# Performance work log

Measured on AMD Instinct MI355X. Metric: run time of the kernel, lower is better.

Reference implementation:

```python
import jax, jax.numpy as jnp
import numpy as np

B, T, N, FIN = 32, 12, 1024, 64
K, OUT_F = 3, 64


def setup_inputs() -> dict:
    key = jax.random.key(0)
    k1, k2, k3 = jax.random.split(key, 3)
    x = jax.random.normal(k1, (B, T, N, FIN), dtype=jnp.float32)
    A = jax.random.uniform(k2, (B, N, N), dtype=jnp.float32)
    # Xavier-uniform-like init for Theta [K, in_f, out_f]
    limit = float(np.sqrt(6.0 / (FIN + OUT_F)))
    Theta = jax.random.uniform(k3, (K, FIN, OUT_F), dtype=jnp.float32,
                               minval=-limit, maxval=limit)
    return {"x": x, "A": A, "Theta": Theta}


def reference(x, A, Theta):
    Bb, Tt, Nn, Fin = x.shape
    Kk = Theta.shape[0]
    I = jnp.broadcast_to(jnp.eye(Nn, dtype=x.dtype), (Bb, Nn, Nn))
    # lambda_max = max row-sum of A, clamped to >= 1
    lambda_max = jnp.maximum(jnp.max(jnp.sum(A, axis=-1), axis=-1), 1.0)
    L = 2.0 * A / lambda_max[:, None, None] - I  # scaled Laplacian surrogate [B,N,N]
    out = jnp.zeros((Bb, Tt, Nn, Theta.shape[-1]), dtype=x.dtype)
    T_prev2, T_prev = None, I
    for k in range(Kk):  # small fixed K-hop loop
        if k == 0:
            T_k = I
        elif k == 1:
            T_k = L
        else:
            T_k = 2.0 * jnp.einsum('bnm,bmp->bnp', L, T_prev) - T_prev2
        T_prev2, T_prev = T_prev, T_k
        rhs = jnp.einsum('btnf,fo->btno', x, Theta[k])   # feature transform
        out = out + jnp.einsum('bnm,btmo->btno', T_k, rhs)  # graph aggregation
    return jax.nn.relu(out)
```

## Files before the change

### kernel.cpp

```cpp
#include <hip/hip_runtime.h>

typedef unsigned short ushort_t;
typedef unsigned char uchar_t;
typedef __attribute__((ext_vector_type(8))) __bf16 bf16x8;
typedef __attribute__((ext_vector_type(4))) float f32x4;
typedef __attribute__((ext_vector_type(8))) unsigned short u16x8;
typedef __attribute__((ext_vector_type(8))) int i32x8;

#define NB 32
#define TT 12
#define NNODE 1024
#define FF 64
#define OO 64
#define TO 768

#define SCL_ONE 127
#define SCL_E   118

__device__ __forceinline__ unsigned short f2bf(float f) {
    unsigned u = __float_as_uint(f);
    u += 0x7FFFu + ((u >> 16) & 1u);
    return (unsigned short)(u >> 16);
}
__device__ __forceinline__ float bf2f(unsigned short h) {
    return __uint_as_float(((unsigned)h) << 16);
}
__device__ __forceinline__ unsigned char f2fp8(float f) {
    return (unsigned char)(__builtin_amdgcn_cvt_pk_fp8_f32(f, f, 0, false) & 0xff);
}

__device__ __forceinline__ void gload16(const void* g, void* l) {
    __builtin_amdgcn_global_load_lds(
        (const __attribute__((address_space(1))) unsigned int*)g,
        (__attribute__((address_space(3))) unsigned int*)l, 16, 0, 0);
}

__global__ void k_init(unsigned* lam) {
    if (threadIdx.x < NB) lam[threadIdx.x] = 0x3F800000u;
}

__global__ __launch_bounds__(256) void k_rowmax(const float* __restrict__ A,
                                                unsigned* __restrict__ lam) {
    const int b = blockIdx.x >> 4;
    const int chunk = blockIdx.x & 15;
    const int w = threadIdx.x >> 6, lane = threadIdx.x & 63;
    const float* Ab = A + (size_t)b * NNODE * NNODE;
    float mx = 0.0f;
    for (int r = 0; r < 16; ++r) {
        const float* rp = Ab + (size_t)(chunk * 64 + w * 16 + r) * NNODE;
        float s = 0.0f;
#pragma unroll
        for (int j = 0; j < 16; ++j) s += rp[lane + j * 64];
#pragma unroll
        for (int off = 32; off > 0; off >>= 1) s += __shfl_down(s, off, 64);
        if (lane == 0) mx = fmaxf(mx, s);
    }
    if (lane == 0) atomicMax(&lam[b], __float_as_uint(mx));
}

__global__ __launch_bounds__(256) void k_escale(const float* __restrict__ A,
                                                const unsigned* __restrict__ lam,
                                                uchar_t* __restrict__ E8) {
    const size_t idx = ((size_t)blockIdx.x * 256 + threadIdx.x) * 8;
    const int b = (int)(idx >> 20);
    const float scl = 1024.0f / __uint_as_float(lam[b]);
    const float4 v0 = *(const float4*)(A + idx);
    const float4 v1 = *(const float4*)(A + idx + 4);
    unsigned lo = 0, hi = 0;
    lo = (unsigned)__builtin_amdgcn_cvt_pk_fp8_f32(v0.x * scl, v0.y * scl, (int)lo, false);
    lo = (unsigned)__builtin_amdgcn_cvt_pk_fp8_f32(v0.z * scl, v0.w * scl, (int)lo, true);
    hi = (unsigned)__builtin_amdgcn_cvt_pk_fp8_f32(v1.x * scl, v1.y * scl, (int)hi, false);
    hi = (unsigned)__builtin_amdgcn_cvt_pk_fp8_f32(v1.z * scl, v1.w * scl, (int)hi, true);
    uint2 pk; pk.x = lo; pk.y = hi;
    *(uint2*)(E8 + idx) = pk;
}

__global__ void k_theta(const float* __restrict__ Th, ushort_t* __restrict__ Tht) {
    int tid = blockIdx.x * 256 + threadIdx.x;
    if (tid < 3 * 64 * 64) {
        int k = tid >> 12, rem = tid & 4095, o = rem >> 6, f = rem & 63;
        Tht[tid] = f2bf(Th[(k << 12) + (f << 6) + o]);
    }
}

__global__ __launch_bounds__(256) void k_feature(const float* __restrict__ x,
                                                 const ushort_t* __restrict__ Tht,
                                                 ushort_t* __restrict__ Pb,
                                                 ushort_t* __restrict__ Qc,
                                                 uchar_t* __restrict__ R2f8) {
    __shared__ ushort_t xt[128 * 64];
    __shared__ ushort_t tb[64 * 136];
    const int n0 = blockIdx.x * 128;
    const int t = blockIdx.y;
    const int b = blockIdx.z;
    const int tid = threadIdx.x;
    const int w = tid >> 6, lane = tid & 63, quad = lane >> 4, l15 = lane & 15;

    const float* xb = x + (((size_t)b * TT + t) * NNODE + n0) * FF;
#pragma unroll
    for (int i = 0; i < 8; ++i) {
        int q = i * 256 + tid;
        int row = q >> 4, fq = q & 15;
        const float4 v = *(const float4*)(xb + row * 64 + fq * 4);
        uint2 pk;
        pk.x = (unsigned)f2bf(v.x) | ((unsigned)f2bf(v.y) << 16);
        pk.y = (unsigned)f2bf(v.z) | ((unsigned)f2bf(v.w) << 16);
        *(uint2*)(xt + row * 64 + fq * 4) = pk;
    }
    __syncthreads();

    bf16x8 af[2][2];
#pragma unroll
    for (int rb = 0; rb < 2; ++rb)
#pragma unroll
        for (int ks = 0; ks < 2; ++ks)
            af[rb][ks] = *(const bf16x8*)(xt + (w * 32 + rb * 16 + l15) * 64 + ks * 32 + quad * 8);

    f32x4 acc[3][2][4];
#pragma unroll
    for (int k = 0; k < 3; ++k)
#pragma unroll
        for (int rb = 0; rb < 2; ++rb)
#pragma unroll
            for (int cb = 0; cb < 4; ++cb)
                acc[k][rb][cb] = (f32x4){0.f, 0.f, 0.f, 0.f};

#pragma unroll
    for (int k = 0; k < 3; ++k)
#pragma unroll
        for (int ks = 0; ks < 2; ++ks)
#pragma unroll
            for (int cb = 0; cb < 4; ++cb) {
                bf16x8 bfr = *(const bf16x8*)(Tht + ((size_t)(k * 64 + cb * 16 + l15)) * 64 + ks * 32 + quad * 8);
#pragma unroll
                for (int rb = 0; rb < 2; ++rb)
                    acc[k][rb][cb] = __builtin_amdgcn_mfma_f32_16x16x32_bf16(af[rb][ks], bfr, acc[k][rb][cb], 0, 0, 0);
            }

    ushort_t* Pbb = Pb + (((size_t)b * TT + t) * NNODE + n0) * OO;
#pragma unroll
    for (int rb = 0; rb < 2; ++rb)
#pragma unroll
        for (int cb = 0; cb < 4; ++cb)
#pragma unroll
            for (int r = 0; r < 4; ++r) {
                int n = w * 32 + rb * 16 + quad * 4 + r;
                int o = cb * 16 + l15;
                Pbb[(size_t)n * OO + o] = f2bf(acc[0][rb][cb][r] - acc[2][rb][cb][r]);
            }

    {
#pragma unroll
        for (int rb = 0; rb < 2; ++rb)
#pragma unroll
            for (int cb = 0; cb < 4; ++cb)
#pragma unroll
                for (int r = 0; r < 4; ++r) {
                    int nl = w * 32 + rb * 16 + quad * 4 + r;
                    int o = cb * 16 + l15;
                    tb[o * 136 + nl] = f2bf(acc[1][rb][cb][r] - 2.0f * acc[2][rb][cb][r]);
                }
        __syncthreads();
        int o = tid >> 2, seg = tid & 3;
        ushort_t* drow = Qc + ((size_t)b * TO + t * 64 + o) * NNODE + n0 + seg * 32;
        const ushort_t* srow = tb + o * 136 + seg * 32;
#pragma unroll
        for (int i = 0; i < 4; ++i)
            *(u16x8*)(drow + i * 8) = *(const u16x8*)(srow + i * 8);
        __syncthreads();
    }
    {
        char* tbc = (char*)tb;
#pragma unroll
        for (int rb = 0; rb < 2; ++rb)
#pragma unroll
            for (int cb = 0; cb < 4; ++cb)
#pragma unroll
                for (int r = 0; r < 4; ++r) {
                    int nl = w * 32 + rb * 16 + quad * 4 + r;
                    int o = cb * 16 + l15;
                    tbc[o * 144 + nl] = (char)f2fp8(acc[2][rb][cb][r]);
                }
        __syncthreads();
        int o = tid >> 2, seg = tid & 3;
        uchar_t* drow = R2f8 + ((size_t)b * TO + t * 64 + o) * NNODE + n0 + seg * 32;
        const char* srow = tbc + o * 144 + seg * 32;
        *(int4*)(drow) = *(const int4*)(srow);
        *(int4*)(drow + 16) = *(const int4*)(srow + 16);
    }
}

template <int MODE>
__global__ __launch_bounds__(256) void k_gemm8(const uchar_t* __restrict__ Aop, size_t aBS,
                                               const uchar_t* __restrict__ Bop, size_t bBS,
                                               const ushort_t* __restrict__ Qc,
                                               uchar_t* __restrict__ Zf8,
                                               ushort_t* __restrict__ Pbp,
                                               float* __restrict__ outp) {
    __shared__ __align__(16) uchar_t smem[34816];
    uchar_t* At = smem;
    uchar_t* Bt = smem + 16384;
    const int bid = blockIdx.x;
    const int xcd = bid & 7, y = bid >> 3;
    const int tile = y % 48;
    const int b = xcd + 8 * (y / 48);
    const int tm = (MODE == 1) ? (tile >> 3) : (tile / 6);
    const int tn = (MODE == 1) ? (tile & 7) : (tile % 6);
    const int m0 = tm * 128, n0 = tn * 128;
    const int tid = threadIdx.x;
    const int w = tid >> 6, lane = tid & 63, quad = lane >> 4, l15 = lane & 15;
    const int wr = w >> 1, wc = w & 1;
    const uchar_t* Ab = Aop + (size_t)b * aBS + (size_t)m0 * NNODE;
    const uchar_t* Bb = Bop + (size_t)b * bBS + (size_t)n0 * NNODE;

    int ldso[4];
    size_t goff[4];
#pragma unroll
    for (int i = 0; i < 4; ++i) {
        int slot = i * 256 + tid;
        int row = slot >> 3;
        int lc = (slot & 7) ^ (row & 7);
        ldso[i] = slot * 16;
        goff[i] = (size_t)row * NNODE + lc * 16;
    }

    f32x4 acc[4][4];
#pragma unroll
    for (int i = 0; i < 4; ++i)
#pragma unroll
        for (int j = 0; j < 4; ++j) acc[i][j] = (f32x4){0.f, 0.f, 0.f, 0.f};

    for (int kk = 0; kk < 8; ++kk) {
        const int k0 = kk << 7;
#pragma unroll
        for (int i = 0; i < 4; ++i) {
            gload16(Ab + k0 + goff[i], At + ldso[i]);
            gload16(Bb + k0 + goff[i], Bt + ldso[i]);
        }
        __syncthreads();
        i32x8 af[4], bfr[4];
#pragma unroll
        for (int i = 0; i < 4; ++i) {
            const int m = wr * 64 + i * 16 + l15;
            const int n = wc * 64 + i * 16 + l15;
            const int4 alo = *(const int4*)(At + m * 128 + (((quad << 1)) ^ (m & 7)) * 16);
            const int4 ahi = *(const int4*)(At + m * 128 + (((quad << 1) | 1) ^ (m & 7)) * 16);
            const int4 blo = *(const int4*)(Bt + n * 128 + (((quad << 1)) ^ (n & 7)) * 16);
            const int4 bhi = *(const int4*)(Bt + n * 128 + (((quad << 1) | 1) ^ (n & 7)) * 16);
            af[i] = (i32x8){alo.x, alo.y, alo.z, alo.w, ahi.x, ahi.y, ahi.z, ahi.w};
            bfr[i] = (i32x8){blo.x, blo.y, blo.z, blo.w, bhi.x, bhi.y, bhi.z, bhi.w};
        }
#pragma unroll
        for (int i = 0; i < 4; ++i)
#pragma unroll
            for (int j = 0; j < 4; ++j)
                acc[i][j] = __builtin_amdgcn_mfma_scale_f32_16x16x128_f8f6f4(
                    af[i], bfr[j], acc[i][j], 0, 0, 0, SCL_ONE, 0, SCL_E);
        __syncthreads();
    }

    if (MODE == 1) {
        ushort_t* tb = (ushort_t*)smem;
        const ushort_t* Qb = Qc + (size_t)b * TO * NNODE;
        uchar_t* Zb = Zf8 + (size_t)b * TO * NNODE;
#pragma unroll
        for (int i = 0; i < 4; ++i)
#pragma unroll
            for (int r = 0; r < 4; ++r) {
                const int cl = wr * 64 + i * 16 + quad * 4 + r;
                const int c = m0 + cl;
#pragma unroll
                for (int j = 0; j < 4; ++j) {
                    const int nl = wc * 64 + j * 16 + l15;
                    const size_t zi = (size_t)c * NNODE + n0 + nl;
                    const float z = bf2f(Qb[zi]) + 2.0f * acc[i][j][r];
                    Zb[zi] = f2fp8(z);
                    tb[nl * 136 + cl] = f2bf(z);
                }
            }
        __syncthreads();
        const int t0 = m0 >> 6;
        const int row = tid >> 1, half = tid & 1;
        ushort_t* prow = Pbp + (((size_t)b * TT + t0 + half) * NNODE + n0 + row) * OO;
        const ushort_t* srow = tb + row * 136 + half * 64;
#pragma unroll
        for (int s = 0; s < 8; ++s) {
            u16x8 pv = *(const u16x8*)(prow + s * 8);
            u16x8 zv = *(const u16x8*)(srow + s * 8);
            u16x8 rv;
#pragma unroll
            for (int e = 0; e < 8; ++e) rv[e] = f2bf(bf2f(pv[e]) - bf2f(zv[e]));
            *(u16x8*)(prow + s * 8) = rv;
        }
    } else {
#pragma unroll
        for (int i = 0; i < 4; ++i)
#pragma unroll
            for (int r = 0; r < 4; ++r) {
                const int n = m0 + wr * 64 + i * 16 + quad * 4 + r;
#pragma unroll
                for (int j = 0; j < 4; ++j) {
                    const int c = n0 + wc * 64 + j * 16 + l15;
                    const int t = c >> 6, o = c & 63;
                    const size_t id = (((size_t)b * TT + t) * NNODE + n) * OO + o;
                    outp[id] = fmaxf(bf2f(Pbp[id]) + acc[i][j][r], 0.0f);
                }
            }
    }
}

extern "C" void kernel_launch(void* const* d_in, const int* in_sizes, int n_in,
                              void* d_out, int out_size, void* d_ws, size_t ws_size,
                              hipStream_t stream) {
    const float* x = (const float*)d_in[0];
    const float* A = (const float*)d_in[1];
    const float* Th = (const float*)d_in[2];
    float* out = (float*)d_out;
    char* ws = (char*)d_ws;

    unsigned* lam = (unsigned*)ws;
    uchar_t* E8 = (uchar_t*)(ws + 256);
    uchar_t* R2f8 = E8 + (size_t)NB * NNODE * NNODE;
    uchar_t* Zf8 = R2f8 + (size_t)NB * TO * NNODE;
    ushort_t* Qc = (ushort_t*)(Zf8 + (size_t)NB * TO * NNODE);
    ushort_t* Pb = Qc + (size_t)NB * TO * NNODE;
    ushort_t* Tht = Pb + (size_t)NB * TT * NNODE * OO;

    k_init<<<1, 64, 0, stream>>>(lam);
    k_rowmax<<<512, 256, 0, stream>>>(A, lam);
    k_escale<<<16384, 256, 0, stream>>>(A, lam, E8);
    k_theta<<<48, 256, 0, stream>>>(Th, Tht);
    k_feature<<<dim3(8, 12, 32), 256, 0, stream>>>(x, Tht, Pb, Qc, R2f8);
    k_gemm8<1><<<1536, 256, 0, stream>>>(R2f8, (size_t)TO * NNODE,
                                         E8, (size_t)NNODE * NNODE,
                                         Qc, Zf8, Pb, nullptr);
    k_gemm8<2><<<1536, 256, 0, stream>>>(E8, (size_t)NNODE * NNODE,
                                         Zf8, (size_t)TO * NNODE,
                                         nullptr, nullptr, Pb, out);
}
```

Measured before the change: 496.5 us.

## Restructure feature kernel: 512 threads, Theta staged in swizzled LDS, merged epilogue

The feature-transform kernel now runs 512 threads per block, and each wave handles 16 rows instead of 32. x is read straight from global into MFMA fragments, with no LDS staging. Theta is staged in LDS with an XOR swizzle rather than read per fragment from global. The Qc and R2 transposes share one LDS buffer region and a single barrier, removing two syncs. This aims for more parallelism and fewer barriers in a memory-bound kernel, at the cost of fewer MFMAs per Theta fragment load.

```diff
diff --git a/kernel.cpp b/kernel.cpp
--- a/kernel.cpp
+++ b/kernel.cpp
@@ -83,110 +83,91 @@
     }
 }
 
-__global__ __launch_bounds__(256) void k_feature(const float* __restrict__ x,
-                                                 const ushort_t* __restrict__ Tht,
-                                                 ushort_t* __restrict__ Pb,
-                                                 ushort_t* __restrict__ Qc,
-                                                 uchar_t* __restrict__ R2f8) {
-    __shared__ ushort_t xt[128 * 64];
-    __shared__ ushort_t tb[64 * 136];
+__global__ __launch_bounds__(512, 5) void k_feature(const float* __restrict__ x,
+                                                    const ushort_t* __restrict__ Tht,
+                                                    ushort_t* __restrict__ Pb,
+                                                    ushort_t* __restrict__ Qc,
+                                                    uchar_t* __restrict__ R2f8) {
+    __shared__ __align__(16) uchar_t th[3 * 64 * 128];
+    __shared__ __align__(16) uchar_t tbuf[26624];
+    ushort_t* tbq = (ushort_t*)tbuf;
+    char* tbr = (char*)(tbuf + 17408);
+
     const int n0 = blockIdx.x * 128;
     const int t = blockIdx.y;
     const int b = blockIdx.z;
     const int tid = threadIdx.x;
     const int w = tid >> 6, lane = tid & 63, quad = lane >> 4, l15 = lane & 15;
 
-    const float* xb = x + (((size_t)b * TT + t) * NNODE + n0) * FF;
-#pragma unroll
-    for (int i = 0; i < 8; ++i) {
-        int q = i * 256 + tid;
-        int row = q >> 4, fq = q & 15;
-        const float4 v = *(const float4*)(xb + row * 64 + fq * 4);
-        uint2 pk;
-        pk.x = (unsigned)f2bf(v.x) | ((unsigned)f2bf(v.y) << 16);
-        pk.y = (unsigned)f2bf(v.z) | ((unsigned)f2bf(v.w) << 16);
-        *(uint2*)(xt + row * 64 + fq * 4) = pk;
+#pragma unroll
+    for (int i = 0; i < 3; ++i) {
+        int chunk = i * 512 + tid;
+        int ko = chunk >> 3, c = chunk & 7;
+        int phys = c ^ (ko & 7);
+        const int4 v = *(const int4*)(Tht + ko * 64 + c * 8);
+        *(int4*)(th + ko * 128 + phys * 16) = v;
+    }
+
+    const float* xr = x + (((size_t)b * TT + t) * NNODE + n0 + w * 16 + l15) * FF;
+    bf16x8 af[2];
+#pragma unroll
+    for (int ks = 0; ks < 2; ++ks) {
+        const float4 v0 = *(const float4*)(xr + ks * 32 + quad * 8);
+        const float4 v1 = *(const float4*)(xr + ks * 32 + quad * 8 + 4);
+        u16x8 p;
+        p[0] = f2bf(v0.x); p[1] = f2bf(v0.y); p[2] = f2bf(v0.z); p[3] = f2bf(v0.w);
+        p[4] = f2bf(v1.x); p[5] = f2bf(v1.y); p[6] = f2bf(v1.z); p[7] = f2bf(v1.w);
+        af[ks] = *(bf16x8*)&p;
     }
     __syncthreads();
 
-    bf16x8 af[2][2];
-#pragma unroll
-    for (int rb = 0; rb < 2; ++rb)
+    f32x4 acc[3][4];
+#pragma unroll
+    for (int k = 0; k < 3; ++k)
+#pragma unroll
+        for (int cb = 0; cb < 4; ++cb) acc[k][cb] = (f32x4){0.f, 0.f, 0.f, 0.f};
+
+#pragma unroll
+    for (int k = 0; k < 3; ++k)
 #pragma unroll
         for (int ks = 0; ks < 2; ++ks)
-            af[rb][ks] = *(const bf16x8*)(xt + (w * 32 + rb * 16 + l15) * 64 + ks * 32 + quad * 8);
-
-    f32x4 acc[3][2][4];
-#pragma unroll
-    for (int k = 0; k < 3; ++k)
-#pragma unroll
-        for (int rb = 0; rb < 2; ++rb)
-#pragma unroll
-            for (int cb = 0; cb < 4; ++cb)
-                acc[k][rb][cb] = (f32x4){0.f, 0.f, 0.f, 0.f};
-
-#pragma unroll
-    for (int k = 0; k < 3; ++k)
-#pragma unroll
-        for (int ks = 0; ks < 2; ++ks)
 #pragma unroll
             for (int cb = 0; cb < 4; ++cb) {
-                bf16x8 bfr = *(const bf16x8*)(Tht + ((size_t)(k * 64 + cb * 16 + l15)) * 64 + ks * 32 + quad * 8);
-#pragma unroll
-                for (int rb = 0; rb < 2; ++rb)
-                    acc[k][rb][cb] = __builtin_amdgcn_mfma_f32_16x16x32_bf16(af[rb][ks], bfr, acc[k][rb][cb], 0, 0, 0);
+                const int o = cb * 16 + l15;
+                const int c = (ks * 4 + quad) ^ (o & 7);
+                const bf16x8 bfr = *(const bf16x8*)(th + (k * 64 + o) * 128 + c * 16);
+                acc[k][cb] = __builtin_amdgcn_mfma_f32_16x16x32_bf16(af[ks], bfr, acc[k][cb], 0, 0, 0);
             }
 
     ushort_t* Pbb = Pb + (((size_t)b * TT + t) * NNODE + n0) * OO;
 #pragma unroll
-    for (int rb = 0; rb < 2; ++rb)
-#pragma unroll
-        for (int cb = 0; cb < 4; ++cb)
-#pragma unroll
-            for (int r = 0; r < 4; ++r) {
-                int n = w * 32 + rb * 16 + quad * 4 + r;
-                int o = cb * 16 + l15;
-                Pbb[(size_t)n * OO + o] = f2bf(acc[0][rb][cb][r] - acc[2][rb][cb][r]);
-            }
+    for (int cb = 0; cb < 4; ++cb)
+#pragma unroll
+        for (int r = 0; r < 4; ++r) {
+            const int n = w * 16 + quad * 4 + r;
+            const int o = cb * 16 + l15;
+            Pbb[(size_t)n * OO + o] = f2bf(acc[0][cb][r] - acc[2][cb][r]);
+        }
+
+#pragma unroll
+    for (int cb = 0; cb < 4; ++cb)
+#pragma unroll
+        for (int r = 0; r < 4; ++r) {
+            const int nl = w * 16 + quad * 4 + r;
+            const int o = cb * 16 + l15;
+            tbq[o * 136 + nl] = f2bf(acc[1][cb][r] - 2.0f * acc[2][cb][r]);
+            tbr[o * 144 + nl] = (char)f2fp8(acc[2][cb][r]);
+        }
+    __syncthreads();
 
     {
-#pragma unroll
-        for (int rb = 0; rb < 2; ++rb)
-#pragma unroll
-            for (int cb = 0; cb < 4; ++cb)
-#pragma unroll
-                for (int r = 0; r < 4; ++r) {
-                    int nl = w * 32 + rb * 16 + quad * 4 + r;
-                    int o = cb * 16 + l15;
-                    tb[o * 136 + nl] = f2bf(acc[1][rb][cb][r] - 2.0f * acc[2][rb][cb][r]);
-                }
-        __syncthreads();
-        int o = tid >> 2, seg = tid & 3;
-        ushort_t* drow = Qc + ((size_t)b * TO + t * 64 + o) * NNODE + n0 + seg * 32;
-        const ushort_t* srow = tb + o * 136 + seg * 32;
-#pragma unroll
-        for (int i = 0; i < 4; ++i)
-            *(u16x8*)(drow + i * 8) = *(const u16x8*)(srow + i * 8);
-        __syncthreads();
-    }
-    {
-        char* tbc = (char*)tb;
-#pragma unroll
-        for (int rb = 0; rb < 2; ++rb)
-#pragma unroll
-            for (int cb = 0; cb < 4; ++cb)
-#pragma unroll
-                for (int r = 0; r < 4; ++r) {
-                    int nl = w * 32 + rb * 16 + quad * 4 + r;
-                    int o = cb * 16 + l15;
-                    tbc[o * 144 + nl] = (char)f2fp8(acc[2][rb][cb][r]);
-                }
-        __syncthreads();
-        int o = tid >> 2, seg = tid & 3;
-        uchar_t* drow = R2f8 + ((size_t)b * TO + t * 64 + o) * NNODE + n0 + seg * 32;
-        const char* srow = tbc + o * 144 + seg * 32;
-        *(int4*)(drow) = *(const int4*)(srow);
-        *(int4*)(drow + 16) = *(const int4*)(srow + 16);
+        const int o = tid >> 3, seg = tid & 7;
+        ushort_t* qrow = Qc + ((size_t)b * TO + t * 64 + o) * NNODE + n0 + seg * 16;
+        const ushort_t* sq = tbq + o * 136 + seg * 16;
+        *(u16x8*)(qrow) = *(const u16x8*)(sq);
+        *(u16x8*)(qrow + 8) = *(const u16x8*)(sq + 8);
+        uchar_t* rrow = R2f8 + ((size_t)b * TO + t * 64 + o) * NNODE + n0 + seg * 16;
+        *(int4*)rrow = *(const int4*)(tbr + o * 144 + seg * 16);
     }
 }
 
@@ -330,7 +311,7 @@
     k_rowmax<<<512, 256, 0, stream>>>(A, lam);
     k_escale<<<16384, 256, 0, stream>>>(A, lam, E8);
     k_theta<<<48, 256, 0, stream>>>(Th, Tht);
-    k_feature<<<dim3(8, 12, 32), 256, 0, stream>>>(x, Tht, Pb, Qc, R2f8);
+    k_feature<<<dim3(8, 12, 32), 512, 0, stream>>>(x, Tht, Pb, Qc, R2f8);
     k_gemm8<1><<<1536, 256, 0, stream>>>(R2f8, (size_t)TO * NNODE,
                                          E8, (size_t)NNODE * NNODE,
                                          Qc, Zf8, Pb, nullptr);
```

Result: faster. 465.6 us (-6.2%).
